# Kernel optimization log

Hardware: AMD Instinct MI355X
Metric: run time of the kernel (lower is better)

The kernel has to match this reference:

```python
import jax, jax.numpy as jnp
import numpy as np

K = 3      # kernel_size
S = 2      # stride
EPS = 1e-5 # BatchNorm eps


def setup_inputs() -> dict:
    key = jax.random.key(0)
    ks = jax.random.split(key, 6)
    B, C, H, W = 8, 256, 128, 128
    k2 = K * K
    return {
        "x": jax.random.normal(ks[0], (B, C, H, W), jnp.float32),
        "w_conv": jax.random.normal(ks[1], (k2, C, K, K), jnp.float32) * 0.05,
        "bn_gamma": jnp.ones((k2,), jnp.float32),
        "bn_beta": jnp.zeros((k2,), jnp.float32),
        "bn_mean": jax.random.normal(ks[2], (k2,), jnp.float32) * 0.1,
        "bn_var": jnp.ones((k2,), jnp.float32),
        "ch_w1": jax.random.normal(ks[3], (C // 4, C), jnp.float32) * 0.05,
        "ch_w2": jax.random.normal(ks[4], (C, C // 4), jnp.float32) * 0.05,
    }


def reference(x, w_conv, bn_gamma, bn_beta, bn_mean, bn_var, ch_w1, ch_w2):
    b, c, h, w = x.shape
    oh = (h - 1) // S + 1
    ow = (w - 1) // S + 1
    # weight_net: strided KxK conv (C -> k2) + eval-mode BatchNorm
    wlog = jax.lax.conv_general_dilated(
        x, w_conv, window_strides=(S, S), padding=((1, 1), (1, 1)),
        dimension_numbers=("NCHW", "OIHW", "NCHW"))  # (b, k2, oh, ow)
    scale = bn_gamma / jnp.sqrt(bn_var + EPS)
    wlog = (wlog - bn_mean[None, :, None, None]) * scale[None, :, None, None] \
        + bn_beta[None, :, None, None]
    # channel_net: GAP -> 1x1 conv -> relu -> 1x1 conv (all bias-free)
    gap = x.mean(axis=(2, 3))                      # (b, c)
    ch = jax.nn.relu(gap @ ch_w1.T) @ ch_w2.T      # (b, c)
    # per-pixel, per-channel logits over the k^2 taps; softmax over taps
    logits = wlog[:, None] * ch[:, :, None, None, None]  # (b, c, k2, oh, ow)
    attn = jax.nn.softmax(logits, axis=2)
    # unfold: reflect pad then KxK patches with stride S (tap order row-major,
    # matching torch unfold(2,.).unfold(3,.) and the k2->(k,k) reshape)
    px = jnp.pad(x, ((0, 0), (0, 0), (1, 1), (1, 1)), mode="reflect")
    taps = []
    for di in range(K):
        for dj in range(K):
            taps.append(px[:, :, di:di + (oh - 1) * S + 1:S,
                           dj:dj + (ow - 1) * S + 1:S])
    patches = jnp.stack(taps, axis=2)              # (b, c, k2, oh, ow)
    return (attn * patches).sum(axis=2)            # (b, c, oh, ow)
```

## Files before the change

### kernel.cpp

```cpp
#include <hip/hip_runtime.h>
#include <hip/hip_bf16.h>


#define EPS 1e-5f
#define CH_SPLIT 8
#define WLOG_N 393216

__global__ __launch_bounds__(256) void prep_kernel(
    const float* __restrict__ wconv, const float* __restrict__ gamma,
    const float* __restrict__ beta, const float* __restrict__ mean,
    const float* __restrict__ var, float* __restrict__ wt,
    float* __restrict__ bias, float* __restrict__ gap) {
  const int blk = blockIdx.x;
  const int c = threadIdx.x;
  if (blk < 9) {
    const int t = blk;
    const float sc = gamma[t] * rsqrtf(var[t] + EPS);
    const float* src = wconv + ((size_t)t * 256 + c) * 9;
    float* dst = wt + c * 84;
    #pragma unroll
    for (int ki = 0; ki < 3; ++ki)
      #pragma unroll
      for (int kj = 0; kj < 3; ++kj)
        dst[ki * 28 + t * 3 + kj] = src[ki * 3 + kj] * sc;
  } else {
    #pragma unroll
    for (int ki = 0; ki < 3; ++ki) wt[c * 84 + ki * 28 + 27] = 0.f;
    #pragma unroll
    for (int k = 0; k < 8; ++k) gap[k * 256 + c] = 0.f;
    if (c < 9) bias[c] = beta[c] - mean[c] * gamma[c] * rsqrtf(var[c] + EPS);
    else if (c < 16) bias[c] = 0.f;
  }
}

__global__ __launch_bounds__(256, 2) void conv_kernel(
    const float* __restrict__ x, const float* __restrict__ wt,
    float* __restrict__ wlogp, float* __restrict__ gap) {
  const int j = threadIdx.x & 63;
  const int wv = threadIdx.x >> 6;
  const int i0 = blockIdx.x * 4;
  const int b = blockIdx.y;
  const int z = blockIdx.z;

  __shared__ float sw[2688];
  __shared__ float red[4][64][9];

  {
    const float4* src = (const float4*)(wt + (size_t)z * 32 * 84);
    float4* dst = (float4*)sw;
    #pragma unroll
    for (int k = 0; k < 3; ++k) {
      int idx = k * 256 + threadIdx.x;
      if (idx < 672) dst[idx] = src[idx];
    }
  }
  __syncthreads();

  float acc[4][9];
  #pragma unroll
  for (int ri = 0; ri < 4; ++ri)
    #pragma unroll
    for (int t = 0; t < 9; ++t) acc[ri][t] = 0.f;

  const int cbase = z * 32 + wv * 8;
  const float* xb = x + ((size_t)b * 256 + cbase) * 16384;
  const float* swb = sw + (wv * 8) * 84;
  const int h0 = 2 * i0 - 1;
  const int jl = (j == 0) ? 0 : (2 * j - 1);

  for (int c = 0; c < 8; ++c) {
    const float* xc = xb + (size_t)c * 16384;
    float2 v[9];
    float lf[9];
    #pragma unroll
    for (int r = 0; r < 9; ++r) {
      const int hh = h0 + r;
      if ((unsigned)hh < 128u) {
        v[r] = *(const float2*)(xc + hh * 128 + 2 * j);
        lf[r] = xc[hh * 128 + jl];
      } else {
        v[r] = make_float2(0.f, 0.f);
        lf[r] = 0.f;
      }
    }
    if (j == 0) {
      #pragma unroll
      for (int r = 0; r < 9; ++r) lf[r] = 0.f;
    }

    {
      float gs = 0.f;
      #pragma unroll
      for (int r = 1; r < 9; ++r) gs += v[r].x + v[r].y;
      #pragma unroll
      for (int off = 32; off; off >>= 1) gs += __shfl_xor(gs, off, 64);
      if (j == 0) atomicAdd(&gap[b * 256 + cbase + c], gs);
    }

    const float* wcb = swb + c * 84;
    #pragma unroll
    for (int ki = 0; ki < 3; ++ki) {
      float4 wk[7];
      const float4* wq = (const float4*)(wcb + ki * 28);
      #pragma unroll
      for (int q = 0; q < 7; ++q) wk[q] = wq[q];
      const float* w = (const float*)wk;
      #pragma unroll
      for (int ri = 0; ri < 4; ++ri) {
        const int r = 2 * ri + ki;
        const float x0 = lf[r], x1 = v[r].x, x2 = v[r].y;
        #pragma unroll
        for (int t = 0; t < 9; ++t) {
          float a = acc[ri][t];
          a = fmaf(x0, w[t * 3 + 0], a);
          a = fmaf(x1, w[t * 3 + 1], a);
          a = fmaf(x2, w[t * 3 + 2], a);
          acc[ri][t] = a;
        }
      }
    }
  }

  float* wzp = wlogp + (size_t)z * WLOG_N;
  #pragma unroll
  for (int ri = 0; ri < 4; ++ri) {
    __syncthreads();
    #pragma unroll
    for (int t = 0; t < 9; ++t) red[wv][j][t] = acc[ri][t];
    __syncthreads();
    const size_t rowpos = ((size_t)b * 64 + (i0 + ri)) * 64;
    float* wp = wzp + rowpos * 12;
    for (int idx = threadIdx.x; idx < 768; idx += 256) {
      const int jj = idx / 12, tt = idx - jj * 12;
      float s = 0.f;
      if (tt < 9)
        s = red[0][jj][tt] + red[1][jj][tt] + red[2][jj][tt] + red[3][jj][tt];
      wp[idx] = s;
    }
  }
}

__global__ __launch_bounds__(256) void reduce_chnet_kernel(
    const float* __restrict__ wlogp, const float* __restrict__ bias,
    float* __restrict__ wlog, const float* __restrict__ gap,
    const float* __restrict__ w1, const float* __restrict__ w2,
    float* __restrict__ ch) {
  __shared__ float g[256];
  __shared__ float h[64];
  const int blk = blockIdx.x;
  if (blk < 384) {
    const int i4 = blk * 256 + threadIdx.x;
    float4 s = make_float4(0.f, 0.f, 0.f, 0.f);
    #pragma unroll
    for (int zz = 0; zz < 8; ++zz) {
      float4 p = *(const float4*)(wlogp + (size_t)zz * WLOG_N + (size_t)i4 * 4);
      s.x += p.x; s.y += p.y; s.z += p.z; s.w += p.w;
    }
    const int base = i4 * 4;
    s.x += bias[(base + 0) % 12];
    s.y += bias[(base + 1) % 12];
    s.z += bias[(base + 2) % 12];
    s.w += bias[(base + 3) % 12];
    *(float4*)(wlog + base) = s;
  } else {
    const int b = blk - 384;
    const int t = threadIdx.x;
    g[t] = gap[b * 256 + t] * (1.f / 16384.f);
    __syncthreads();
    if (t < 64) {
      float s = 0.f;
      const float* w = w1 + t * 256;
      for (int c = 0; c < 256; ++c) s += g[c] * w[c];
      h[t] = fmaxf(s, 0.f);
    }
    __syncthreads();
    float s = 0.f;
    const float* w = w2 + t * 64;
    #pragma unroll 4
    for (int jj = 0; jj < 64; ++jj) s += h[jj] * w[jj];
    ch[b * 256 + t] = s;
  }
}

__global__ __launch_bounds__(256) void final_kernel(
    const float* __restrict__ x, const float* __restrict__ wlog,
    const float* __restrict__ ch, float* __restrict__ out) {
  const int q = threadIdx.x & 31;
  const int rw = threadIdx.x >> 5;
  const int i = blockIdx.x * 8 + rw;
  const int b = blockIdx.y;
  const int c0 = blockIdx.z * 8;

  const size_t pos = ((size_t)b * 64 + i) * 64 + 2 * q;
  const float4* wp = (const float4*)(wlog + pos * 12);
  float4 w0 = wp[0], w1 = wp[1], w2 = wp[2];
  float4 w3 = wp[3], w4 = wp[4], w5 = wp[5];
  const float wlA[9] = {w0.x, w0.y, w0.z, w0.w, w1.x, w1.y, w1.z, w1.w, w2.x};
  const float wlB[9] = {w3.x, w3.y, w3.z, w3.w, w4.x, w4.y, w4.z, w4.w, w5.x};

  float mxA = wlA[0], mnA = wlA[0], mxB = wlB[0], mnB = wlB[0];
  #pragma unroll
  for (int t = 1; t < 9; ++t) {
    mxA = fmaxf(mxA, wlA[t]); mnA = fminf(mnA, wlA[t]);
    mxB = fmaxf(mxB, wlB[t]); mnB = fminf(mnB, wlB[t]);
  }

  const float* chp = ch + b * 256 + c0;
  const float* xp0 = x + ((size_t)b * 256 + c0) * 16384 + 4 * q;
  float* op = out + ((size_t)b * 256 + c0) * 4096 + i * 64 + 2 * q;

  const int hm = (i == 0) ? 1 : 2 * i - 1;

  for (int c = 0; c < 8; ++c) {
    const float chv = chp[c];
    const float* xp = xp0 + (size_t)c * 16384;
    float4 v0 = *(const float4*)(xp + hm * 128);
    float4 v1 = *(const float4*)(xp + (2 * i) * 128);
    float4 v2 = *(const float4*)(xp + (2 * i + 1) * 128);

    float l0 = __shfl_up(v0.w, 1, 32);
    float l1 = __shfl_up(v1.w, 1, 32);
    float l2 = __shfl_up(v2.w, 1, 32);
    if (q == 0) { l0 = v0.y; l1 = v1.y; l2 = v2.y; }

    {
      const float m = fmaxf(mxA * chv, mnA * chv);
      float e[9], s = 0.f;
      #pragma unroll
      for (int t = 0; t < 9; ++t) {
        e[t] = __expf(wlA[t] * chv - m);
        s += e[t];
      }
      float acc = e[0] * l0 + e[1] * v0.x + e[2] * v0.y;
      acc += e[3] * l1 + e[4] * v1.x + e[5] * v1.y;
      acc += e[6] * l2 + e[7] * v2.x + e[8] * v2.y;
      op[(size_t)c * 4096] = acc / s;
    }
    {
      const float m = fmaxf(mxB * chv, mnB * chv);
      float e[9], s = 0.f;
      #pragma unroll
      for (int t = 0; t < 9; ++t) {
        e[t] = __expf(wlB[t] * chv - m);
        s += e[t];
      }
      float acc = e[0] * v0.y + e[1] * v0.z + e[2] * v0.w;
      acc += e[3] * v1.y + e[4] * v1.z + e[5] * v1.w;
      acc += e[6] * v2.y + e[7] * v2.z + e[8] * v2.w;
      op[(size_t)c * 4096 + 1] = acc / s;
    }
  }
}

extern "C" void kernel_launch(void* const* d_in, const int* in_sizes, int n_in,
                              void* d_out, int out_size, void* d_ws,
                              size_t ws_size, hipStream_t stream) {
  const float* x = (const float*)d_in[0];
  const float* w_conv = (const float*)d_in[1];
  const float* bn_gamma = (const float*)d_in[2];
  const float* bn_beta = (const float*)d_in[3];
  const float* bn_mean = (const float*)d_in[4];
  const float* bn_var = (const float*)d_in[5];
  const float* ch_w1 = (const float*)d_in[6];
  const float* ch_w2 = (const float*)d_in[7];
  float* out = (float*)d_out;

  float* wsf = (float*)d_ws;
  float* gap = wsf;
  float* ch = wsf + 2048;
  float* bias = wsf + 4096;
  float* wt = wsf + 4112;
  float* wlog = wsf + 25616;
  float* wlogp = wsf + 418832;

  prep_kernel<<<10, 256, 0, stream>>>(w_conv, bn_gamma, bn_beta, bn_mean,
                                      bn_var, wt, bias, gap);
  conv_kernel<<<dim3(16, 8, CH_SPLIT), 256, 0, stream>>>(x, wt, wlogp, gap);
  reduce_chnet_kernel<<<392, 256, 0, stream>>>(wlogp, bias, wlog, gap, ch_w1,
                                               ch_w2, ch);
  final_kernel<<<dim3(8, 8, 32), 256, 0, stream>>>(x, wlog, ch, out);
}
```

Baseline: 79.90 us.

## Retile conv kernel: 512-thread blocks, two output columns per lane, phased LDS reduction

The strided conv kernel now runs 512 threads per block covering 8 output rows. Each lane loads float4 input rows and computes two adjacent output columns for two rows, so the shared middle column is reused and fewer redundant row loads are issued. The cross-channel-group reduction is now done in LDS in four serialized phases, followed by a single coalesced write of all 8 rows. This trades more loads per thread for fewer blocks, and the phased accumulation adds barriers and serial LDS work.

```diff
diff --git a/kernel.cpp b/kernel.cpp
--- a/kernel.cpp
+++ b/kernel.cpp
@@ -33,68 +33,76 @@
   }
 }
 
-__global__ __launch_bounds__(256, 2) void conv_kernel(
+__global__ __launch_bounds__(512, 2) void conv_kernel(
     const float* __restrict__ x, const float* __restrict__ wt,
     float* __restrict__ wlogp, float* __restrict__ gap) {
-  const int j = threadIdx.x & 63;
+  const int l = threadIdx.x & 63;
+  const int q = l & 31;
+  const int sh = l >> 5;
   const int wv = threadIdx.x >> 6;
-  const int i0 = blockIdx.x * 4;
+  const int rg = wv & 1;
+  const int cg = wv >> 1;
+  const int i0 = blockIdx.x * 8;
   const int b = blockIdx.y;
   const int z = blockIdx.z;
 
   __shared__ float sw[2688];
-  __shared__ float red[4][64][9];
+  __shared__ float red[8][65][9];
 
   {
     const float4* src = (const float4*)(wt + (size_t)z * 32 * 84);
     float4* dst = (float4*)sw;
     #pragma unroll
-    for (int k = 0; k < 3; ++k) {
-      int idx = k * 256 + threadIdx.x;
+    for (int k = 0; k < 2; ++k) {
+      int idx = k * 512 + threadIdx.x;
       if (idx < 672) dst[idx] = src[idx];
     }
   }
   __syncthreads();
 
-  float acc[4][9];
+  float acc[2][2][9];
   #pragma unroll
-  for (int ri = 0; ri < 4; ++ri)
-    #pragma unroll
-    for (int t = 0; t < 9; ++t) acc[ri][t] = 0.f;
-
-  const int cbase = z * 32 + wv * 8;
+  for (int ro = 0; ro < 2; ++ro)
+    #pragma unroll
+    for (int cp = 0; cp < 2; ++cp)
+      #pragma unroll
+      for (int t = 0; t < 9; ++t) acc[ro][cp][t] = 0.f;
+
+  const int cbase = z * 32 + cg * 8;
   const float* xb = x + ((size_t)b * 256 + cbase) * 16384;
-  const float* swb = sw + (wv * 8) * 84;
-  const int h0 = 2 * i0 - 1;
-  const int jl = (j == 0) ? 0 : (2 * j - 1);
+  const float* swb = sw + (cg * 8) * 84;
+  const int iA0 = i0 + rg * 4 + sh * 2;
+  const int h0 = 2 * iA0 - 1;
+  const int jl = (q == 0) ? 0 : (4 * q - 1);
 
   for (int c = 0; c < 8; ++c) {
     const float* xc = xb + (size_t)c * 16384;
-    float2 v[9];
-    float lf[9];
-    #pragma unroll
-    for (int r = 0; r < 9; ++r) {
+    float4 v[5];
+    float lf[5];
+    #pragma unroll
+    for (int r = 0; r < 5; ++r) {
       const int hh = h0 + r;
       if ((unsigned)hh < 128u) {
-        v[r] = *(const float2*)(xc + hh * 128 + 2 * j);
+        v[r] = *(const float4*)(xc + hh * 128 + 4 * q);
         lf[r] = xc[hh * 128 + jl];
       } else {
-        v[r] = make_float2(0.f, 0.f);
+        v[r] = make_float4(0.f, 0.f, 0.f, 0.f);
         lf[r] = 0.f;
       }
     }
-    if (j == 0) {
-      #pragma unroll
-      for (int r = 0; r < 9; ++r) lf[r] = 0.f;
+    if (q == 0) {
+      #pragma unroll
+      for (int r = 0; r < 5; ++r) lf[r] = 0.f;
     }
 
     {
       float gs = 0.f;
       #pragma unroll
-      for (int r = 1; r < 9; ++r) gs += v[r].x + v[r].y;
+      for (int r = 1; r < 5; ++r)
+        gs += (v[r].x + v[r].y) + (v[r].z + v[r].w);
       #pragma unroll
       for (int off = 32; off; off >>= 1) gs += __shfl_xor(gs, off, 64);
-      if (j == 0) atomicAdd(&gap[b * 256 + cbase + c], gs);
+      if (l == 0) atomicAdd(&gap[b * 256 + cbase + c], gs);
     }
 
     const float* wcb = swb + c * 84;
@@ -103,40 +111,56 @@
       float4 wk[7];
       const float4* wq = (const float4*)(wcb + ki * 28);
       #pragma unroll
-      for (int q = 0; q < 7; ++q) wk[q] = wq[q];
+      for (int p = 0; p < 7; ++p) wk[p] = wq[p];
       const float* w = (const float*)wk;
       #pragma unroll
-      for (int ri = 0; ri < 4; ++ri) {
-        const int r = 2 * ri + ki;
-        const float x0 = lf[r], x1 = v[r].x, x2 = v[r].y;
+      for (int ro = 0; ro < 2; ++ro) {
+        const int r = 2 * ro + ki;
+        const float xA0 = lf[r], xA1 = v[r].x, xA2 = v[r].y;
+        const float xB1 = v[r].z, xB2 = v[r].w;
         #pragma unroll
         for (int t = 0; t < 9; ++t) {
-          float a = acc[ri][t];
-          a = fmaf(x0, w[t * 3 + 0], a);
-          a = fmaf(x1, w[t * 3 + 1], a);
-          a = fmaf(x2, w[t * 3 + 2], a);
-          acc[ri][t] = a;
+          float a = acc[ro][0][t];
+          a = fmaf(xA0, w[t * 3 + 0], a);
+          a = fmaf(xA1, w[t * 3 + 1], a);
+          a = fmaf(xA2, w[t * 3 + 2], a);
+          acc[ro][0][t] = a;
+          float bacc = acc[ro][1][t];
+          bacc = fmaf(xA2, w[t * 3 + 0], bacc);
+          bacc = fmaf(xB1, w[t * 3 + 1], bacc);
+          bacc = fmaf(xB2, w[t * 3 + 2], bacc);
+          acc[ro][1][t] = bacc;
         }
       }
     }
   }
 
+  const int row0 = rg * 4 + sh * 2;
+  #pragma unroll
+  for (int phase = 0; phase < 4; ++phase) {
+    if (cg == phase) {
+      #pragma unroll
+      for (int ro = 0; ro < 2; ++ro)
+        #pragma unroll
+        for (int cp = 0; cp < 2; ++cp)
+          #pragma unroll
+          for (int t = 0; t < 9; ++t) {
+            if (phase == 0)
+              red[row0 + ro][2 * q + cp][t] = acc[ro][cp][t];
+            else
+              red[row0 + ro][2 * q + cp][t] += acc[ro][cp][t];
+          }
+    }
+    __syncthreads();
+  }
+
   float* wzp = wlogp + (size_t)z * WLOG_N;
-  #pragma unroll
-  for (int ri = 0; ri < 4; ++ri) {
-    __syncthreads();
-    #pragma unroll
-    for (int t = 0; t < 9; ++t) red[wv][j][t] = acc[ri][t];
-    __syncthreads();
-    const size_t rowpos = ((size_t)b * 64 + (i0 + ri)) * 64;
-    float* wp = wzp + rowpos * 12;
-    for (int idx = threadIdx.x; idx < 768; idx += 256) {
-      const int jj = idx / 12, tt = idx - jj * 12;
-      float s = 0.f;
-      if (tt < 9)
-        s = red[0][jj][tt] + red[1][jj][tt] + red[2][jj][tt] + red[3][jj][tt];
-      wp[idx] = s;
-    }
+  for (int idx = threadIdx.x; idx < 8 * 768; idx += 512) {
+    const int row = idx / 768;
+    const int rem = idx - row * 768;
+    const int jj = rem / 12, tt = rem - jj * 12;
+    const float s = (tt < 9) ? red[row][jj][tt] : 0.f;
+    wzp[((size_t)(b * 64 + i0 + row) * 64 + jj) * 12 + tt] = s;
   }
 }
 
@@ -275,7 +299,7 @@
 
   prep_kernel<<<10, 256, 0, stream>>>(w_conv, bn_gamma, bn_beta, bn_mean,
                                       bn_var, wt, bias, gap);
-  conv_kernel<<<dim3(16, 8, CH_SPLIT), 256, 0, stream>>>(x, wt, wlogp, gap);
+  conv_kernel<<<dim3(8, 8, CH_SPLIT), 512, 0, stream>>>(x, wt, wlogp, gap);
   reduce_chnet_kernel<<<392, 256, 0, stream>>>(wlogp, bias, wlog, gap, ch_w1,
                                                ch_w2, ch);
   final_kernel<<<dim3(8, 8, 32), 256, 0, stream>>>(x, wlog, ch, out);
```

After: 106.6 us. 1.33x slower.

## Restructure conv kernel to stage input rows in LDS with double buffering

Applied to the files above, without the earlier changes.

The conv kernel now has each wave own one output row and loop over all 32 channels, instead of splitting channels across waves and reducing partial sums through shared memory. Input rows for each channel are loaded cooperatively as float4 into a double-buffered LDS tile, with the next channel prefetched while the current one is computed. GAP partial sums are gathered in LDS and written with one global atomic per channel. This removes the cross-wave reduction and the redundant scalar global loads, at the cost of one barrier per channel and LDS atomics.

```diff
diff --git a/kernel.cpp b/kernel.cpp
--- a/kernel.cpp
+++ b/kernel.cpp
@@ -36,107 +36,113 @@
 __global__ __launch_bounds__(256, 2) void conv_kernel(
     const float* __restrict__ x, const float* __restrict__ wt,
     float* __restrict__ wlogp, float* __restrict__ gap) {
-  const int j = threadIdx.x & 63;
-  const int wv = threadIdx.x >> 6;
+  const int tid = threadIdx.x;
+  const int j = tid & 63;
+  const int ri = tid >> 6;
   const int i0 = blockIdx.x * 4;
   const int b = blockIdx.y;
   const int z = blockIdx.z;
 
   __shared__ float sw[2688];
-  __shared__ float red[4][64][9];
+  __shared__ float xs[2][9][128];
+  __shared__ float gap_lds[32];
 
   {
     const float4* src = (const float4*)(wt + (size_t)z * 32 * 84);
     float4* dst = (float4*)sw;
     #pragma unroll
     for (int k = 0; k < 3; ++k) {
-      int idx = k * 256 + threadIdx.x;
+      int idx = k * 256 + tid;
       if (idx < 672) dst[idx] = src[idx];
     }
   }
+  if (tid < 32) gap_lds[tid] = 0.f;
   __syncthreads();
 
-  float acc[4][9];
+  const float* xb = x + ((size_t)b * 256 + (size_t)z * 32) * 16384;
+  const int h0 = 2 * i0 - 1;
+
+  const int rf0 = tid >> 5;
+  const int c40 = tid & 31;
+  const int hh0 = h0 + rf0;
+  const bool ok0 = (unsigned)hh0 < 128u;
+  const bool do1 = tid < 32;
+  const int hh1 = h0 + 8;
+
+  float acc[9];
   #pragma unroll
-  for (int ri = 0; ri < 4; ++ri)
-    #pragma unroll
-    for (int t = 0; t < 9; ++t) acc[ri][t] = 0.f;
-
-  const int cbase = z * 32 + wv * 8;
-  const float* xb = x + ((size_t)b * 256 + cbase) * 16384;
-  const float* swb = sw + (wv * 8) * 84;
-  const int h0 = 2 * i0 - 1;
-  const int jl = (j == 0) ? 0 : (2 * j - 1);
-
-  for (int c = 0; c < 8; ++c) {
-    const float* xc = xb + (size_t)c * 16384;
-    float2 v[9];
-    float lf[9];
-    #pragma unroll
-    for (int r = 0; r < 9; ++r) {
-      const int hh = h0 + r;
-      if ((unsigned)hh < 128u) {
-        v[r] = *(const float2*)(xc + hh * 128 + 2 * j);
-        lf[r] = xc[hh * 128 + jl];
-      } else {
-        v[r] = make_float2(0.f, 0.f);
-        lf[r] = 0.f;
-      }
-    }
-    if (j == 0) {
-      #pragma unroll
-      for (int r = 0; r < 9; ++r) lf[r] = 0.f;
-    }
-
-    {
-      float gs = 0.f;
-      #pragma unroll
-      for (int r = 1; r < 9; ++r) gs += v[r].x + v[r].y;
-      #pragma unroll
-      for (int off = 32; off; off >>= 1) gs += __shfl_xor(gs, off, 64);
-      if (j == 0) atomicAdd(&gap[b * 256 + cbase + c], gs);
-    }
-
-    const float* wcb = swb + c * 84;
+  for (int t = 0; t < 9; ++t) acc[t] = 0.f;
+
+  {
+    const float* xc = xb;
+    float4 s0 = ok0 ? *(const float4*)(xc + hh0 * 128 + c40 * 4)
+                    : make_float4(0.f, 0.f, 0.f, 0.f);
+    float4 s1 = make_float4(0.f, 0.f, 0.f, 0.f);
+    if (do1) s1 = *(const float4*)(xc + hh1 * 128 + c40 * 4);
+    float gs = 0.f;
+    if (rf0 >= 1) gs += (s0.x + s0.y) + (s0.z + s0.w);
+    gs += (s1.x + s1.y) + (s1.z + s1.w);
+    atomicAdd(&gap_lds[0], gs);
+    float4* base = (float4*)&xs[0][0][0];
+    base[tid] = s0;
+    if (do1) base[256 + tid] = s1;
+  }
+
+  for (int c = 0; c < 32; ++c) {
+    __syncthreads();
+    const int bf = c & 1;
+
+    float4 s0 = make_float4(0.f, 0.f, 0.f, 0.f);
+    float4 s1 = make_float4(0.f, 0.f, 0.f, 0.f);
+    const bool pf = (c < 31);
+    if (pf) {
+      const float* xc = xb + (size_t)(c + 1) * 16384;
+      if (ok0) s0 = *(const float4*)(xc + hh0 * 128 + c40 * 4);
+      if (do1) s1 = *(const float4*)(xc + hh1 * 128 + c40 * 4);
+    }
+
+    const float* wcb = sw + c * 84;
     #pragma unroll
     for (int ki = 0; ki < 3; ++ki) {
       float4 wk[7];
       const float4* wq = (const float4*)(wcb + ki * 28);
       #pragma unroll
-      for (int q = 0; q < 7; ++q) wk[q] = wq[q];
+      for (int p = 0; p < 7; ++p) wk[p] = wq[p];
       const float* w = (const float*)wk;
-      #pragma unroll
-      for (int ri = 0; ri < 4; ++ri) {
-        const int r = 2 * ri + ki;
-        const float x0 = lf[r], x1 = v[r].x, x2 = v[r].y;
-        #pragma unroll
-        for (int t = 0; t < 9; ++t) {
-          float a = acc[ri][t];
-          a = fmaf(x0, w[t * 3 + 0], a);
-          a = fmaf(x1, w[t * 3 + 1], a);
-          a = fmaf(x2, w[t * 3 + 2], a);
-          acc[ri][t] = a;
-        }
+      const int r = 2 * ri + ki;
+      const float2 v = *(const float2*)&xs[bf][r][2 * j];
+      const float lf = (j == 0) ? 0.f : xs[bf][r][2 * j - 1];
+      #pragma unroll
+      for (int t = 0; t < 9; ++t) {
+        float a = acc[t];
+        a = fmaf(lf, w[t * 3 + 0], a);
+        a = fmaf(v.x, w[t * 3 + 1], a);
+        a = fmaf(v.y, w[t * 3 + 2], a);
+        acc[t] = a;
       }
     }
-  }
-
-  float* wzp = wlogp + (size_t)z * WLOG_N;
-  #pragma unroll
-  for (int ri = 0; ri < 4; ++ri) {
-    __syncthreads();
-    #pragma unroll
-    for (int t = 0; t < 9; ++t) red[wv][j][t] = acc[ri][t];
-    __syncthreads();
-    const size_t rowpos = ((size_t)b * 64 + (i0 + ri)) * 64;
-    float* wp = wzp + rowpos * 12;
-    for (int idx = threadIdx.x; idx < 768; idx += 256) {
-      const int jj = idx / 12, tt = idx - jj * 12;
-      float s = 0.f;
-      if (tt < 9)
-        s = red[0][jj][tt] + red[1][jj][tt] + red[2][jj][tt] + red[3][jj][tt];
-      wp[idx] = s;
-    }
+
+    if (pf) {
+      float gs = 0.f;
+      if (rf0 >= 1) gs += (s0.x + s0.y) + (s0.z + s0.w);
+      gs += (s1.x + s1.y) + (s1.z + s1.w);
+      atomicAdd(&gap_lds[c + 1], gs);
+      float4* base = (float4*)&xs[bf ^ 1][0][0];
+      base[tid] = s0;
+      if (do1) base[256 + tid] = s1;
+    }
+  }
+
+  __syncthreads();
+  if (tid < 32) atomicAdd(&gap[b * 256 + z * 32 + tid], gap_lds[tid]);
+
+  {
+    float* wzp = wlogp + (size_t)z * WLOG_N;
+    const size_t pos = ((size_t)b * 64 + (i0 + ri)) * 64 + j;
+    float4* wp = (float4*)(wzp + pos * 12);
+    wp[0] = make_float4(acc[0], acc[1], acc[2], acc[3]);
+    wp[1] = make_float4(acc[4], acc[5], acc[6], acc[7]);
+    wp[2] = make_float4(acc[8], 0.f, 0.f, 0.f);
   }
 }
 
```

Result: slower. 161.8 us (+102.5%).
